# Optimization experiments

Hardware: AMD Instinct MI355X
Metric: run time of the kernel (lower is better)

The kernel has to match this reference:

```python
import jax, jax.numpy as jnp
import numpy as np

B, S, D, H = 2, 2048, 2048, 16
HD = D // H
SCALE = 1.0 / np.sqrt(HD)


def setup_inputs() -> dict:
    key = jax.random.key(0)
    ks = jax.random.split(key, 11)
    xav = np.sqrt(6.0 / (D + D))  # xavier uniform bound for square weights
    def w(k):
        return jax.random.uniform(k, (D, D), jnp.float32, -xav, xav)
    return {
        "query": jax.random.normal(ks[0], (B, S, D), jnp.float32),
        "key": jax.random.normal(ks[1], (B, S, D), jnp.float32),
        "value": jax.random.normal(ks[2], (B, S, D), jnp.float32),
        "Wq": w(ks[3]), "bq": jnp.zeros((D,), jnp.float32),
        "Wk": w(ks[4]), "bk": jnp.zeros((D,), jnp.float32),
        "Wv": w(ks[5]), "bv": jnp.zeros((D,), jnp.float32),
        "Wo": w(ks[6]), "bo": jnp.zeros((D,), jnp.float32),
    }


def reference(query, key, value, Wq, bq, Wk, bk, Wv, bv, Wo, bo):
    # projections (torch Linear: x @ W.T + b)
    q = query @ Wq.T + bq
    k = key @ Wk.T + bk
    v = value @ Wv.T + bv
    # [B, H, S, HD]
    q = q.reshape(B, S, H, HD).transpose(0, 2, 1, 3)
    k = k.reshape(B, S, H, HD).transpose(0, 2, 1, 3)
    v = v.reshape(B, S, H, HD).transpose(0, 2, 1, 3)
    scores = jnp.einsum("bhqd,bhkd->bhqk", q, k) * SCALE
    causal = jnp.triu(jnp.ones((S, S), bool), k=1)
    scores = jnp.where(causal, -jnp.inf, scores)
    attn = jax.nn.softmax(scores, axis=-1)  # dropout p=0.0 -> identity
    out = jnp.einsum("bhqk,bhkd->bhqd", attn, v)
    out = out.transpose(0, 2, 1, 3).reshape(B, S, D)
    return out @ Wo.T + bo
```

## Files before the change

### kernel.cpp

```cpp
#include <hip/hip_runtime.h>
#include <hip/hip_bf16.h>


#define LOG2E 1.44269504088896340736f

typedef __attribute__((ext_vector_type(8))) short short8;
typedef __attribute__((ext_vector_type(4))) short short4b;
typedef __attribute__((ext_vector_type(4))) float floatx4;

__device__ __forceinline__ short f2bf(float f) {
  unsigned int u = __builtin_bit_cast(unsigned int, f);
  u += 0x7FFFu + ((u >> 16) & 1u);
  return (short)(u >> 16);
}

__device__ __forceinline__ short4b pack4bf(float a, float b, float c, float d) {
  __hip_bfloat162 lo = __float22bfloat162_rn(float2{a, b});
  __hip_bfloat162 hi = __float22bfloat162_rn(float2{c, d});
  short4b r;
  r[0] = __builtin_bit_cast(short, lo.x); r[1] = __builtin_bit_cast(short, lo.y);
  r[2] = __builtin_bit_cast(short, hi.x); r[3] = __builtin_bit_cast(short, hi.y);
  return r;
}

__device__ __forceinline__ void gl_lds16(const void* g, void* l) {
  __builtin_amdgcn_global_load_lds(
      (const __attribute__((address_space(1))) unsigned int*)g,
      (__attribute__((address_space(3))) unsigned int*)l, 16, 0, 0);
}

__global__ __launch_bounds__(256) void cvt_k(
    const float* __restrict__ s0, const float* __restrict__ s1,
    const float* __restrict__ s2, const float* __restrict__ s3,
    unsigned short* __restrict__ d0, unsigned short* __restrict__ d1,
    unsigned short* __restrict__ d2, unsigned short* __restrict__ d3, int n)
{
  const float* s; unsigned short* d;
  switch (blockIdx.y) {
    case 0: s = s0; d = d0; break;
    case 1: s = s1; d = d1; break;
    case 2: s = s2; d = d2; break;
    default: s = s3; d = d3; break;
  }
  const int i = (blockIdx.x * 256 + threadIdx.x) * 8;
  if (i >= n) return;
  float4 a = *(const float4*)(s + i);
  float4 b = *(const float4*)(s + i + 4);
  short8 v = (short8){f2bf(a.x), f2bf(a.y), f2bf(a.z), f2bf(a.w),
                      f2bf(b.x), f2bf(b.y), f2bf(b.z), f2bf(b.w)};
  *(short8*)(d + i) = v;
}

template<bool OUT_BF16, bool VT_OUT>
__global__ __launch_bounds__(256, 2) void gemm_bf16_k(
    const unsigned short* __restrict__ A, const unsigned short* __restrict__ Bt,
    const float* __restrict__ bias, void* __restrict__ Cptr,
    int M, int N, int K, float alpha)
{
  __shared__ __align__(16) unsigned short smem[VT_OUT ? 128 * 136 : 128 * 64];
  unsigned short* As = smem;
  unsigned short* Bs = smem + 128 * 32;

  const int tid  = threadIdx.x;
  const int lane = tid & 63;
  const int wave = tid >> 6;
  const int quad = lane >> 4;
  const int l16  = lane & 15;
  const int wr   = wave >> 1, wc = wave & 1;
  const long bm  = (long)blockIdx.y * 128;
  const long bn  = (long)blockIdx.x * 128;

  const unsigned short* agp[2]; const unsigned short* bgp[2];
  unsigned short* alp[2]; unsigned short* blp[2];
#pragma unroll
  for (int j = 0; j < 2; ++j) {
    const int p = (wave * 2 + j) * 64 + lane;
    const int r = p >> 2, cs = p & 3;
    const int cg = cs ^ ((r >> 1) & 3);
    agp[j] = A  + (bm + r) * (long)K + cg * 8;
    bgp[j] = Bt + (bn + r) * (long)K + cg * 8;
    alp[j] = As + p * 8;
    blp[j] = Bs + p * 8;
  }

  floatx4 acc[4][4];
#pragma unroll
  for (int i = 0; i < 4; ++i)
#pragma unroll
    for (int j = 0; j < 4; ++j) acc[i][j] = (floatx4){0.f, 0.f, 0.f, 0.f};

  const int coff = (quad ^ ((l16 >> 1) & 3)) * 8;

  for (int k0 = 0; k0 < K; k0 += 32) {
    __syncthreads();
    gl_lds16(agp[0] + k0, alp[0]);
    gl_lds16(agp[1] + k0, alp[1]);
    gl_lds16(bgp[0] + k0, blp[0]);
    gl_lds16(bgp[1] + k0, blp[1]);
    __syncthreads();

    short8 af[4], bf[4];
#pragma unroll
    for (int t = 0; t < 4; ++t) {
      af[t] = *(const short8*)&As[(wr * 64 + t * 16 + l16) * 32 + coff];
      bf[t] = *(const short8*)&Bs[(wc * 64 + t * 16 + l16) * 32 + coff];
    }
#pragma unroll
    for (int mt = 0; mt < 4; ++mt)
#pragma unroll
      for (int nt = 0; nt < 4; ++nt)
        acc[mt][nt] = __builtin_amdgcn_mfma_f32_16x16x32_bf16(af[mt], bf[nt], acc[mt][nt], 0, 0, 0);
  }

  if (VT_OUT) {
    __syncthreads();
    unsigned short* Ct = smem;
#pragma unroll
    for (int nt = 0; nt < 4; ++nt) {
      const long col = bn + wc * 64 + nt * 16 + l16;
      const float bval = bias[col];
      const int col_l = wc * 64 + nt * 16 + l16;
#pragma unroll
      for (int mt = 0; mt < 4; ++mt) {
        const int row_l = wr * 64 + mt * 16 + quad * 4;
#pragma unroll
        for (int rg = 0; rg < 4; ++rg)
          Ct[col_l * 136 + row_l + rg] = (unsigned short)f2bf((acc[mt][nt][rg] + bval) * alpha);
      }
    }
    __syncthreads();
    const int b  = (int)(bm >> 11);
    const int s0 = (int)(bm & 2047);
    const int r    = tid >> 1;
    const int half = tid & 1;
    unsigned short* dst = (unsigned short*)Cptr +
        ((long)(b * 16 + blockIdx.x) * 128 + r) * 2048 + s0 + half * 64;
    const unsigned short* src = &Ct[r * 136 + half * 64];
#pragma unroll
    for (int c = 0; c < 8; ++c)
      *(uint4*)(dst + c * 8) = *(const uint4*)(src + c * 8);
  } else {
#pragma unroll
    for (int nt = 0; nt < 4; ++nt) {
      const long col = bn + wc * 64 + nt * 16 + l16;
      const float bval = bias[col];
#pragma unroll
      for (int mt = 0; mt < 4; ++mt) {
#pragma unroll
        for (int rg = 0; rg < 4; ++rg) {
          const long row = bm + wr * 64 + mt * 16 + quad * 4 + rg;
          const float v = (acc[mt][nt][rg] + bval) * alpha;
          if (OUT_BF16) ((unsigned short*)Cptr)[row * (long)N + col] = (unsigned short)f2bf(v);
          else          ((float*)Cptr)[row * (long)N + col] = v;
        }
      }
    }
  }
}

template<bool A_BF16, bool OUT_BF16, bool VT_OUT>
__global__ __launch_bounds__(256, 2) void gemm_bias_k(
    const void* __restrict__ Aptr, const float* __restrict__ Bt,
    const float* __restrict__ bias, void* __restrict__ Cptr,
    int M, int N, int K, float alpha)
{
  __shared__ __align__(16) unsigned short smem[128 * 136];
  unsigned short* As = smem;
  unsigned short* Bs = smem + 128 * 40;

  const int tid  = threadIdx.x;
  const int lane = tid & 63;
  const int wave = tid >> 6;
  const int quad = lane >> 4;
  const int l16  = lane & 15;
  const int wr   = wave >> 1, wc = wave & 1;
  const long bm  = (long)blockIdx.y * 128;
  const long bn  = (long)blockIdx.x * 128;

  floatx4 acc[4][4];
#pragma unroll
  for (int i = 0; i < 4; ++i)
#pragma unroll
    for (int j = 0; j < 4; ++j) acc[i][j] = (floatx4){0.f, 0.f, 0.f, 0.f};

  const int srow = tid >> 2;
  const int cc   = tid & 3;

  for (int k0 = 0; k0 < K; k0 += 32) {
    __syncthreads();
#pragma unroll
    for (int r = 0; r < 2; ++r) {
      const int row = srow + r * 64;
      short8 av, bv;
      if (A_BF16) {
        av = *(const short8*)((const unsigned short*)Aptr + (bm + row) * (long)K + k0 + cc * 8);
      } else {
        const float* ap = (const float*)Aptr + (bm + row) * (long)K + k0 + cc * 8;
        float4 f0 = *(const float4*)ap;
        float4 f1 = *(const float4*)(ap + 4);
        av = (short8){f2bf(f0.x), f2bf(f0.y), f2bf(f0.z), f2bf(f0.w),
                      f2bf(f1.x), f2bf(f1.y), f2bf(f1.z), f2bf(f1.w)};
      }
      {
        const float* bp = Bt + (bn + row) * (long)K + k0 + cc * 8;
        float4 g0 = *(const float4*)bp;
        float4 g1 = *(const float4*)(bp + 4);
        bv = (short8){f2bf(g0.x), f2bf(g0.y), f2bf(g0.z), f2bf(g0.w),
                      f2bf(g1.x), f2bf(g1.y), f2bf(g1.z), f2bf(g1.w)};
      }
      *(short8*)&As[row * 40 + cc * 8] = av;
      *(short8*)&Bs[row * 40 + cc * 8] = bv;
    }
    __syncthreads();

    short8 af[4], bf[4];
#pragma unroll
    for (int t = 0; t < 4; ++t) {
      af[t] = *(const short8*)&As[(wr * 64 + t * 16 + l16) * 40 + quad * 8];
      bf[t] = *(const short8*)&Bs[(wc * 64 + t * 16 + l16) * 40 + quad * 8];
    }
#pragma unroll
    for (int mt = 0; mt < 4; ++mt)
#pragma unroll
      for (int nt = 0; nt < 4; ++nt)
        acc[mt][nt] = __builtin_amdgcn_mfma_f32_16x16x32_bf16(af[mt], bf[nt], acc[mt][nt], 0, 0, 0);
  }

  if (VT_OUT) {
    __syncthreads();
    unsigned short* Ct = smem;
#pragma unroll
    for (int nt = 0; nt < 4; ++nt) {
      const long col = bn + wc * 64 + nt * 16 + l16;
      const float bval = bias[col];
      const int col_l = wc * 64 + nt * 16 + l16;
#pragma unroll
      for (int mt = 0; mt < 4; ++mt) {
        const int row_l = wr * 64 + mt * 16 + quad * 4;
#pragma unroll
        for (int rg = 0; rg < 4; ++rg)
          Ct[col_l * 136 + row_l + rg] = (unsigned short)f2bf((acc[mt][nt][rg] + bval) * alpha);
      }
    }
    __syncthreads();
    const int b  = (int)(bm >> 11);
    const int s0 = (int)(bm & 2047);
    const int r    = tid >> 1;
    const int half = tid & 1;
    unsigned short* dst = (unsigned short*)Cptr +
        ((long)(b * 16 + blockIdx.x) * 128 + r) * 2048 + s0 + half * 64;
    const unsigned short* src = &Ct[r * 136 + half * 64];
#pragma unroll
    for (int c = 0; c < 8; ++c)
      *(uint4*)(dst + c * 8) = *(const uint4*)(src + c * 8);
  } else {
#pragma unroll
    for (int nt = 0; nt < 4; ++nt) {
      const long col = bn + wc * 64 + nt * 16 + l16;
      const float bval = bias[col];
#pragma unroll
      for (int mt = 0; mt < 4; ++mt) {
#pragma unroll
        for (int rg = 0; rg < 4; ++rg) {
          const long row = bm + wr * 64 + mt * 16 + quad * 4 + rg;
          const float v = (acc[mt][nt][rg] + bval) * alpha;
          if (OUT_BF16) ((unsigned short*)Cptr)[row * (long)N + col] = (unsigned short)f2bf(v);
          else          ((float*)Cptr)[row * (long)N + col] = v;
        }
      }
    }
  }
}

__global__ __launch_bounds__(256, 2) void flash_attn_k(
    const unsigned short* __restrict__ Q,
    const unsigned short* __restrict__ Kp,
    const unsigned short* __restrict__ Vt,
    unsigned short* __restrict__ O)
{
  constexpr int S = 2048, D = 2048, HD = 128;
  constexpr int PS = 72;

  __shared__ __align__(16) unsigned short Ks[64 * 128];
  __shared__ __align__(16) unsigned short Vst[128 * 64];
  __shared__ __align__(16) unsigned short Ps[64 * PS];

  const int tid  = threadIdx.x;
  const int lane = tid & 63;
  const int w    = tid >> 6;
  const int quad = lane >> 4;
  const int l16  = lane & 15;
  const int lx7  = l16 & 7;

  const int bh = blockIdx.y;
  const long headoff = (long)(bh >> 4) * S * D + (long)(bh & 15) * HD;
  const long vtoff   = (long)bh * HD * S;

  const unsigned short* gK[4]; unsigned short* lK[4];
  const unsigned short* gV[4]; unsigned short* lV[4];
#pragma unroll
  for (int i = 0; i < 4; ++i) {
    const int p = (w * 4 + i) * 64 + lane;
    { const int r = p >> 4, cp = p & 15, c = cp ^ (r & 7);
      gK[i] = Kp + headoff + (long)r * D + c * 8;  lK[i] = &Ks[p * 8]; }
    { const int r = p >> 3, cp = p & 7, c = cp ^ (r & 7);
      gV[i] = Vt + vtoff + (long)r * S + c * 8;    lV[i] = &Vst[p * 8]; }
  }

#pragma unroll 1
  for (int half = 0; half < 2; ++half) {
    const int qt = half ? (31 - (int)blockIdx.x) : (int)blockIdx.x;
    const int qbase = qt * 64;
    const int qrow  = qbase + w * 16 + l16;
    const int qloc  = w * 16 + l16;

    short8 aq[4];
    {
      const unsigned short* qp = Q + headoff + (long)qrow * D;
#pragma unroll
      for (int ks = 0; ks < 4; ++ks)
        aq[ks] = *(const short8*)(qp + ks * 32 + quad * 8);
    }

    floatx4 o_acc[8];
#pragma unroll
    for (int t = 0; t < 8; ++t) o_acc[t] = (floatx4){0.f, 0.f, 0.f, 0.f};
    float m_i = -INFINITY, l_i = 0.f;

    for (int kt = 0; kt <= qt; ++kt) {
      const int kbase = kt * 64;
      __syncthreads();
#pragma unroll
      for (int i = 0; i < 4; ++i) gl_lds16(gK[i] + (long)kbase * D, lK[i]);
#pragma unroll
      for (int i = 0; i < 4; ++i) gl_lds16(gV[i] + kbase, lV[i]);
      __syncthreads();

      floatx4 sc[4];
#pragma unroll
      for (int nt = 0; nt < 4; ++nt) sc[nt] = (floatx4){0.f, 0.f, 0.f, 0.f};
#pragma unroll
      for (int nt = 0; nt < 4; ++nt) {
        const int krow = nt * 16 + l16;
#pragma unroll
        for (int ks = 0; ks < 4; ++ks) {
          const int cp = (ks * 4 + quad) ^ lx7;
          short8 kf = *(const short8*)&Ks[krow * 128 + cp * 8];
          sc[nt] = __builtin_amdgcn_mfma_f32_16x16x32_bf16(kf, aq[ks], sc[nt], 0, 0, 0);
        }
      }

      float sv[4][4];
      float rmax = -INFINITY;
      if (kt == qt) {
        const int kg0 = kbase + quad * 4;
#pragma unroll
        for (int nt = 0; nt < 4; ++nt)
#pragma unroll
          for (int rg = 0; rg < 4; ++rg) {
            float v = sc[nt][rg];
            if (kg0 + nt * 16 + rg > qrow) v = -INFINITY;
            sv[nt][rg] = v;
            rmax = fmaxf(rmax, v);
          }
      } else {
#pragma unroll
        for (int nt = 0; nt < 4; ++nt)
#pragma unroll
          for (int rg = 0; rg < 4; ++rg) {
            sv[nt][rg] = sc[nt][rg];
            rmax = fmaxf(rmax, sc[nt][rg]);
          }
      }
      rmax = fmaxf(rmax, __shfl_xor(rmax, 16));
      rmax = fmaxf(rmax, __shfl_xor(rmax, 32));

      const float mn = fmaxf(m_i, rmax);
      const float al = exp2f(m_i - mn);
      m_i = mn;

      float rsum = 0.f;
#pragma unroll
      for (int nt = 0; nt < 4; ++nt) {
        float p0 = exp2f(sv[nt][0] - mn), p1 = exp2f(sv[nt][1] - mn);
        float p2 = exp2f(sv[nt][2] - mn), p3 = exp2f(sv[nt][3] - mn);
        rsum += (p0 + p1) + (p2 + p3);
        *(short4b*)&Ps[qloc * PS + nt * 16 + quad * 4] = pack4bf(p0, p1, p2, p3);
      }
      rsum += __shfl_xor(rsum, 16);
      rsum += __shfl_xor(rsum, 32);
      l_i = l_i * al + rsum;

      if (__any(al != 1.0f)) {
#pragma unroll
        for (int t = 0; t < 8; ++t)
#pragma unroll
          for (int rg = 0; rg < 4; ++rg) o_acc[t][rg] *= al;
      }

      short8 pf[2];
#pragma unroll
      for (int ks = 0; ks < 2; ++ks)
        pf[ks] = *(const short8*)&Ps[qloc * PS + ks * 32 + quad * 8];

#pragma unroll
      for (int t = 0; t < 8; ++t) {
        const int drow = t * 16 + l16;
#pragma unroll
        for (int ks = 0; ks < 2; ++ks) {
          const int cp = (ks * 4 + quad) ^ lx7;
          short8 vf = *(const short8*)&Vst[drow * 64 + cp * 8];
          o_acc[t] = __builtin_amdgcn_mfma_f32_16x16x32_bf16(vf, pf[ks], o_acc[t], 0, 0, 0);
        }
      }
    }

    const float rl = 1.0f / l_i;
    unsigned short* op = O + headoff + (long)qrow * D;
#pragma unroll
    for (int t = 0; t < 8; ++t) {
      *(short4b*)(op + t * 16 + quad * 4) =
          pack4bf(o_acc[t][0] * rl, o_acc[t][1] * rl, o_acc[t][2] * rl, o_acc[t][3] * rl);
    }
  }
}

extern "C" void kernel_launch(void* const* d_in, const int* in_sizes, int n_in,
                              void* d_out, int out_size, void* d_ws, size_t ws_size,
                              hipStream_t stream) {
  const float* query = (const float*)d_in[0];
  const float* key_  = (const float*)d_in[1];
  const float* value = (const float*)d_in[2];
  const float* Wq = (const float*)d_in[3];
  const float* bq = (const float*)d_in[4];
  const float* Wk = (const float*)d_in[5];
  const float* bk = (const float*)d_in[6];
  const float* Wv = (const float*)d_in[7];
  const float* bv = (const float*)d_in[8];
  const float* Wo = (const float*)d_in[9];
  const float* bo = (const float*)d_in[10];
  float* out = (float*)d_out;

  constexpr int Bz = 2, S = 2048, D = 2048;
  constexpr int M = Bz * S;
  constexpr long NELEM = (long)M * D;
  constexpr long WELEM = (long)D * D;

  const float qscale = 0.08838834764831845f * LOG2E;
  dim3 gridG(D / 128, M / 128);

  const size_t need_full = (size_t)(6 * NELEM + 4 * WELEM) * 2;

  if (ws_size >= need_full) {
    unsigned short* Qp  = (unsigned short*)d_ws;
    unsigned short* Kp  = Qp + NELEM;
    unsigned short* Vt  = Kp + NELEM;
    unsigned short* Xq  = Vt + NELEM;
    unsigned short* Xk  = Xq + NELEM;
    unsigned short* Xv  = Xk + NELEM;
    unsigned short* Wqb = Xv + NELEM;
    unsigned short* Wkb = Wqb + WELEM;
    unsigned short* Wvb = Wkb + WELEM;
    unsigned short* Wob = Wvb + WELEM;
    unsigned short* Oa  = Xq;

    cvt_k<<<dim3(NELEM / (8 * 256), 3), 256, 0, stream>>>(
        query, key_, value, value, Xq, Xk, Xv, Xv, (int)NELEM);
    cvt_k<<<dim3(WELEM / (8 * 256), 4), 256, 0, stream>>>(
        Wq, Wk, Wv, Wo, Wqb, Wkb, Wvb, Wob, (int)WELEM);

    gemm_bf16_k<true, false><<<gridG, 256, 0, stream>>>(Xq, Wqb, bq, Qp, M, D, D, qscale);
    gemm_bf16_k<true, false><<<gridG, 256, 0, stream>>>(Xk, Wkb, bk, Kp, M, D, D, 1.0f);
    gemm_bf16_k<true, true ><<<gridG, 256, 0, stream>>>(Xv, Wvb, bv, Vt, M, D, D, 1.0f);

    flash_attn_k<<<dim3(16, 32), 256, 0, stream>>>(Qp, Kp, Vt, Oa);

    gemm_bf16_k<false, false><<<gridG, 256, 0, stream>>>(Oa, Wob, bo, out, M, D, D, 1.0f);
  } else {
    unsigned short* Qp = (unsigned short*)d_ws;
    unsigned short* Kp = Qp + NELEM;
    unsigned short* Vt = Kp + NELEM;
    unsigned short* Oa = Vt + NELEM;

    gemm_bias_k<false, true, false><<<gridG, 256, 0, stream>>>(query, Wq, bq, Qp, M, D, D, qscale);
    gemm_bias_k<false, true, false><<<gridG, 256, 0, stream>>>(key_,  Wk, bk, Kp, M, D, D, 1.0f);
    gemm_bias_k<false, true, true ><<<gridG, 256, 0, stream>>>(value, Wv, bv, Vt, M, D, D, 1.0f);

    flash_attn_k<<<dim3(16, 32), 256, 0, stream>>>(Qp, Kp, Vt, Oa);

    gemm_bias_k<true, false, false><<<gridG, 256, 0, stream>>>(Oa, Wo, bo, out, M, D, D, 1.0f);
  }
}
```

Before: 468.0 us.

## Replace bf16 GEMM with 8-wave 256x128 triple-buffered pipelined kernel

Replaces the 4-wave 128x128 bf16 GEMM with an 8-wave kernel on 256x128 tiles and K-step 64. It triple-buffers LDS with async global-to-LDS loads issued two stages ahead, interleaved with MFMA phases, and uses s_setprio around the MFMA blocks. This is meant to hide global memory latency and cut per-K barrier overhead in the projection GEMMs. The flash attention grid is also remapped so that blocks from the same head are grouped, which is meant to improve K/V cache reuse. The costs are much higher LDS use (one block per CU) and fragile manual waitcnt accounting.

```diff
diff --git a/kernel.cpp b/kernel.cpp
--- a/kernel.cpp
+++ b/kernel.cpp
@@ -52,35 +52,40 @@
 }
 
 template<bool OUT_BF16, bool VT_OUT>
-__global__ __launch_bounds__(256, 2) void gemm_bf16_k(
+__global__ __launch_bounds__(512, 1) void gemm8_k(
     const unsigned short* __restrict__ A, const unsigned short* __restrict__ Bt,
     const float* __restrict__ bias, void* __restrict__ Cptr,
     int M, int N, int K, float alpha)
 {
-  __shared__ __align__(16) unsigned short smem[VT_OUT ? 128 * 136 : 128 * 64];
-  unsigned short* As = smem;
-  unsigned short* Bs = smem + 128 * 32;
+  __shared__ __align__(16) unsigned short As[3][256 * 64];
+  __shared__ __align__(16) unsigned short Bs[3][128 * 64];
+  (void)M;
 
   const int tid  = threadIdx.x;
   const int lane = tid & 63;
   const int wave = tid >> 6;
   const int quad = lane >> 4;
   const int l16  = lane & 15;
-  const int wr   = wave >> 1, wc = wave & 1;
-  const long bm  = (long)blockIdx.y * 128;
+  const int lx7  = l16 & 7;
+  const int wm   = wave >> 1, wn = wave & 1;
+  const long bm  = (long)blockIdx.y * 256;
   const long bn  = (long)blockIdx.x * 128;
 
-  const unsigned short* agp[2]; const unsigned short* bgp[2];
-  unsigned short* alp[2]; unsigned short* blp[2];
+  const unsigned short* gA[4]; int lAo[4];
+  const unsigned short* gB[2]; int lBo[2];
+#pragma unroll
+  for (int j = 0; j < 4; ++j) {
+    const int pa = ((j >> 1) * 16 + wave * 2 + (j & 1)) * 64 + lane;
+    const int r = pa >> 3, cp = pa & 7, cs = cp ^ (r & 7);
+    gA[j]  = A + (bm + r) * (long)K + cs * 8;
+    lAo[j] = pa * 8;
+  }
 #pragma unroll
   for (int j = 0; j < 2; ++j) {
-    const int p = (wave * 2 + j) * 64 + lane;
-    const int r = p >> 2, cs = p & 3;
-    const int cg = cs ^ ((r >> 1) & 3);
-    agp[j] = A  + (bm + r) * (long)K + cg * 8;
-    bgp[j] = Bt + (bn + r) * (long)K + cg * 8;
-    alp[j] = As + p * 8;
-    blp[j] = Bs + p * 8;
+    const int pb = (wave * 2 + j) * 64 + lane;
+    const int r = pb >> 3, cp = pb & 7, cs = cp ^ (r & 7);
+    gB[j]  = Bt + (bn + r) * (long)K + cs * 8;
+    lBo[j] = pb * 8;
   }
 
   floatx4 acc[4][4];
@@ -89,66 +94,141 @@
 #pragma unroll
     for (int j = 0; j < 4; ++j) acc[i][j] = (floatx4){0.f, 0.f, 0.f, 0.f};
 
-  const int coff = (quad ^ ((l16 >> 1) & 3)) * 8;
-
-  for (int k0 = 0; k0 < K; k0 += 32) {
-    __syncthreads();
-    gl_lds16(agp[0] + k0, alp[0]);
-    gl_lds16(agp[1] + k0, alp[1]);
-    gl_lds16(bgp[0] + k0, blp[0]);
-    gl_lds16(bgp[1] + k0, blp[1]);
-    __syncthreads();
-
-    short8 af[4], bf[4];
-#pragma unroll
-    for (int t = 0; t < 4; ++t) {
-      af[t] = *(const short8*)&As[(wr * 64 + t * 16 + l16) * 32 + coff];
-      bf[t] = *(const short8*)&Bs[(wc * 64 + t * 16 + l16) * 32 + coff];
-    }
+  const int NT = K >> 6;
+
+#pragma unroll
+  for (int j = 0; j < 4; ++j) gl_lds16(gA[j], &As[0][lAo[j]]);
+#pragma unroll
+  for (int j = 0; j < 2; ++j) gl_lds16(gB[j], &Bs[0][lBo[j]]);
+  if (NT > 1) {
+#pragma unroll
+    for (int j = 0; j < 4; ++j) gl_lds16(gA[j] + 64, &As[1][lAo[j]]);
+#pragma unroll
+    for (int j = 0; j < 2; ++j) gl_lds16(gB[j] + 64, &Bs[1][lBo[j]]);
+    asm volatile("s_waitcnt vmcnt(6)" ::: "memory");
+  } else {
+    asm volatile("s_waitcnt vmcnt(0)" ::: "memory");
+  }
+  __builtin_amdgcn_s_barrier();
+
+  int cur = 0;
+  for (int t = 0; t < NT; ++t) {
+    int nx2 = cur + 2; if (nx2 >= 3) nx2 -= 3;
+    const long kk2 = (long)(t + 2) * 64;
+    const bool st  = (t + 2) < NT;
+    const unsigned short* Ab = As[cur];
+    const unsigned short* Bb = Bs[cur];
+
+    short8 af[4][2];
 #pragma unroll
     for (int mt = 0; mt < 4; ++mt)
 #pragma unroll
-      for (int nt = 0; nt < 4; ++nt)
-        acc[mt][nt] = __builtin_amdgcn_mfma_f32_16x16x32_bf16(af[mt], bf[nt], acc[mt][nt], 0, 0, 0);
+      for (int ks = 0; ks < 2; ++ks)
+        af[mt][ks] = *(const short8*)&Ab[(wm * 64 + mt * 16 + l16) * 64 +
+                                         (((ks * 4 + quad) ^ lx7) * 8)];
+    short8 bf0, bf1;
+
+    bf0 = *(const short8*)&Bb[(wn * 64 + l16) * 64 + (((quad) ^ lx7) * 8)];
+    bf1 = *(const short8*)&Bb[(wn * 64 + l16) * 64 + (((4 + quad) ^ lx7) * 8)];
+    if (st) { gl_lds16(gA[0] + kk2, &As[nx2][lAo[0]]);
+              gl_lds16(gA[1] + kk2, &As[nx2][lAo[1]]); }
+    __builtin_amdgcn_s_barrier();
+    asm volatile("s_waitcnt lgkmcnt(0)");
+    __builtin_amdgcn_s_setprio(1);
+#pragma unroll
+    for (int mt = 0; mt < 4; ++mt) {
+      acc[mt][0] = __builtin_amdgcn_mfma_f32_16x16x32_bf16(af[mt][0], bf0, acc[mt][0], 0, 0, 0);
+      acc[mt][0] = __builtin_amdgcn_mfma_f32_16x16x32_bf16(af[mt][1], bf1, acc[mt][0], 0, 0, 0);
+    }
+    __builtin_amdgcn_s_setprio(0);
+    __builtin_amdgcn_s_barrier();
+
+    bf0 = *(const short8*)&Bb[(wn * 64 + 16 + l16) * 64 + (((quad) ^ lx7) * 8)];
+    bf1 = *(const short8*)&Bb[(wn * 64 + 16 + l16) * 64 + (((4 + quad) ^ lx7) * 8)];
+    if (st) { gl_lds16(gA[2] + kk2, &As[nx2][lAo[2]]);
+              gl_lds16(gA[3] + kk2, &As[nx2][lAo[3]]); }
+    __builtin_amdgcn_s_barrier();
+    asm volatile("s_waitcnt lgkmcnt(0)");
+    __builtin_amdgcn_s_setprio(1);
+#pragma unroll
+    for (int mt = 0; mt < 4; ++mt) {
+      acc[mt][1] = __builtin_amdgcn_mfma_f32_16x16x32_bf16(af[mt][0], bf0, acc[mt][1], 0, 0, 0);
+      acc[mt][1] = __builtin_amdgcn_mfma_f32_16x16x32_bf16(af[mt][1], bf1, acc[mt][1], 0, 0, 0);
+    }
+    __builtin_amdgcn_s_setprio(0);
+    __builtin_amdgcn_s_barrier();
+
+    bf0 = *(const short8*)&Bb[(wn * 64 + 32 + l16) * 64 + (((quad) ^ lx7) * 8)];
+    bf1 = *(const short8*)&Bb[(wn * 64 + 32 + l16) * 64 + (((4 + quad) ^ lx7) * 8)];
+    if (st) { gl_lds16(gB[0] + kk2, &Bs[nx2][lBo[0]]);
+              gl_lds16(gB[1] + kk2, &Bs[nx2][lBo[1]]); }
+    __builtin_amdgcn_s_barrier();
+    asm volatile("s_waitcnt lgkmcnt(0)");
+    __builtin_amdgcn_s_setprio(1);
+#pragma unroll
+    for (int mt = 0; mt < 4; ++mt) {
+      acc[mt][2] = __builtin_amdgcn_mfma_f32_16x16x32_bf16(af[mt][0], bf0, acc[mt][2], 0, 0, 0);
+      acc[mt][2] = __builtin_amdgcn_mfma_f32_16x16x32_bf16(af[mt][1], bf1, acc[mt][2], 0, 0, 0);
+    }
+    __builtin_amdgcn_s_setprio(0);
+    __builtin_amdgcn_s_barrier();
+
+    bf0 = *(const short8*)&Bb[(wn * 64 + 48 + l16) * 64 + (((quad) ^ lx7) * 8)];
+    bf1 = *(const short8*)&Bb[(wn * 64 + 48 + l16) * 64 + (((4 + quad) ^ lx7) * 8)];
+    __builtin_amdgcn_s_barrier();
+    asm volatile("s_waitcnt lgkmcnt(0)");
+    __builtin_amdgcn_s_setprio(1);
+#pragma unroll
+    for (int mt = 0; mt < 4; ++mt) {
+      acc[mt][3] = __builtin_amdgcn_mfma_f32_16x16x32_bf16(af[mt][0], bf0, acc[mt][3], 0, 0, 0);
+      acc[mt][3] = __builtin_amdgcn_mfma_f32_16x16x32_bf16(af[mt][1], bf1, acc[mt][3], 0, 0, 0);
+    }
+    __builtin_amdgcn_s_setprio(0);
+    if (t + 1 < NT) {
+      if (st) asm volatile("s_waitcnt vmcnt(6)" ::: "memory");
+      else    asm volatile("s_waitcnt vmcnt(0)" ::: "memory");
+    }
+    __builtin_amdgcn_s_barrier();
+
+    cur = cur + 1 >= 3 ? 0 : cur + 1;
   }
 
   if (VT_OUT) {
     __syncthreads();
-    unsigned short* Ct = smem;
+    unsigned short* Ct = &As[0][0];
 #pragma unroll
     for (int nt = 0; nt < 4; ++nt) {
-      const long col = bn + wc * 64 + nt * 16 + l16;
-      const float bval = bias[col];
-      const int col_l = wc * 64 + nt * 16 + l16;
+      const int col_l = wn * 64 + nt * 16 + l16;
+      const float bval = bias[bn + col_l];
 #pragma unroll
       for (int mt = 0; mt < 4; ++mt) {
-        const int row_l = wr * 64 + mt * 16 + quad * 4;
+        const int row_l = wm * 64 + mt * 16 + quad * 4;
 #pragma unroll
         for (int rg = 0; rg < 4; ++rg)
-          Ct[col_l * 136 + row_l + rg] = (unsigned short)f2bf((acc[mt][nt][rg] + bval) * alpha);
+          Ct[col_l * 264 + row_l + rg] = (unsigned short)f2bf((acc[mt][nt][rg] + bval) * alpha);
       }
     }
     __syncthreads();
     const int b  = (int)(bm >> 11);
     const int s0 = (int)(bm & 2047);
-    const int r    = tid >> 1;
-    const int half = tid & 1;
+    const int d   = tid >> 2;
+    const int seg = tid & 3;
     unsigned short* dst = (unsigned short*)Cptr +
-        ((long)(b * 16 + blockIdx.x) * 128 + r) * 2048 + s0 + half * 64;
-    const unsigned short* src = &Ct[r * 136 + half * 64];
+        ((long)(b * 16 + blockIdx.x) * 128 + d) * 2048 + s0 + seg * 64;
+    const unsigned short* src = &Ct[d * 264 + seg * 64];
 #pragma unroll
     for (int c = 0; c < 8; ++c)
       *(uint4*)(dst + c * 8) = *(const uint4*)(src + c * 8);
   } else {
 #pragma unroll
     for (int nt = 0; nt < 4; ++nt) {
-      const long col = bn + wc * 64 + nt * 16 + l16;
+      const long col = bn + wn * 64 + nt * 16 + l16;
       const float bval = bias[col];
 #pragma unroll
       for (int mt = 0; mt < 4; ++mt) {
 #pragma unroll
         for (int rg = 0; rg < 4; ++rg) {
-          const long row = bm + wr * 64 + mt * 16 + quad * 4 + rg;
+          const long row = bm + wm * 64 + mt * 16 + quad * 4 + rg;
           const float v = (acc[mt][nt][rg] + bval) * alpha;
           if (OUT_BF16) ((unsigned short*)Cptr)[row * (long)N + col] = (unsigned short)f2bf(v);
           else          ((float*)Cptr)[row * (long)N + col] = v;
@@ -292,7 +372,12 @@
   const int l16  = lane & 15;
   const int lx7  = l16 & 7;
 
-  const int bh = blockIdx.y;
+  const int bx  = blockIdx.x;
+  const int by  = blockIdx.y;
+  const int idx = by * 2 + (bx >> 3);
+  const int bh  = (bx & 7) * 4 + (idx >> 4);
+  const int qsel = idx & 15;
+
   const long headoff = (long)(bh >> 4) * S * D + (long)(bh & 15) * HD;
   const long vtoff   = (long)bh * HD * S;
 
@@ -309,7 +394,7 @@
 
 #pragma unroll 1
   for (int half = 0; half < 2; ++half) {
-    const int qt = half ? (31 - (int)blockIdx.x) : (int)blockIdx.x;
+    const int qt = half ? (31 - qsel) : qsel;
     const int qbase = qt * 64;
     const int qrow  = qbase + w * 16 + l16;
     const int qloc  = w * 16 + l16;
@@ -448,6 +533,7 @@
 
   const float qscale = 0.08838834764831845f * LOG2E;
   dim3 gridG(D / 128, M / 128);
+  dim3 gridG8(D / 128, M / 256);
 
   const size_t need_full = (size_t)(6 * NELEM + 4 * WELEM) * 2;
 
@@ -469,13 +555,13 @@
     cvt_k<<<dim3(WELEM / (8 * 256), 4), 256, 0, stream>>>(
         Wq, Wk, Wv, Wo, Wqb, Wkb, Wvb, Wob, (int)WELEM);
 
-    gemm_bf16_k<true, false><<<gridG, 256, 0, stream>>>(Xq, Wqb, bq, Qp, M, D, D, qscale);
-    gemm_bf16_k<true, false><<<gridG, 256, 0, stream>>>(Xk, Wkb, bk, Kp, M, D, D, 1.0f);
-    gemm_bf16_k<true, true ><<<gridG, 256, 0, stream>>>(Xv, Wvb, bv, Vt, M, D, D, 1.0f);
+    gemm8_k<true, false><<<gridG8, 512, 0, stream>>>(Xq, Wqb, bq, Qp, M, D, D, qscale);
+    gemm8_k<true, false><<<gridG8, 512, 0, stream>>>(Xk, Wkb, bk, Kp, M, D, D, 1.0f);
+    gemm8_k<true, true ><<<gridG8, 512, 0, stream>>>(Xv, Wvb, bv, Vt, M, D, D, 1.0f);
 
     flash_attn_k<<<dim3(16, 32), 256, 0, stream>>>(Qp, Kp, Vt, Oa);
 
-    gemm_bf16_k<false, false><<<gridG, 256, 0, stream>>>(Oa, Wob, bo, out, M, D, D, 1.0f);
+    gemm8_k<false, false><<<gridG8, 512, 0, stream>>>(Oa, Wob, bo, out, M, D, D, 1.0f);
   } else {
     unsigned short* Qp = (unsigned short*)d_ws;
     unsigned short* Kp = Qp + NELEM;
```

Result: faster. 458.4 us (-2.0%).
